# Performance work log

Hardware: AMD Instinct MI355X
Metric: run time of the kernel (lower is better)

The kernel has to match this reference:

```python
import jax, jax.numpy as jnp
import numpy as np

H = 1024  # hidden size
E = 512   # embedding size
L = 2     # lstm layers


def _lstm_cell(x, h, c, W_ih, W_hh, b):
    # x:[B,in], h,c:[B,H]; gates in torch order i,f,g,o
    gates = x @ W_ih.T + h @ W_hh.T + b
    i, f, g, o = jnp.split(gates, 4, axis=-1)
    i, f, o = jax.nn.sigmoid(i), jax.nn.sigmoid(f), jax.nn.sigmoid(o)
    g = jnp.tanh(g)
    c_new = f * c + i * g
    h_new = o * jnp.tanh(c_new)
    return h_new, c_new


def setup_inputs() -> dict:
    key = jax.random.key(0)
    ks = jax.random.split(key, 12)
    B, T, S = 32, 50, 100
    s = 0.02
    return {
        "inputs": jax.random.normal(ks[0], (B, T, E), jnp.float32),
        "memory_bank": jax.random.normal(ks[1], (B, S, H), jnp.float32),
        "mask": jnp.ones((B, S), jnp.bool_),
        "h0": jax.random.normal(ks[2], (L, B, H), jnp.float32),
        "c0": jax.random.normal(ks[3], (L, B, H), jnp.float32),
        "W_ih0": jax.random.normal(ks[4], (4 * H, E + H), jnp.float32) * s,
        "W_hh0": jax.random.normal(ks[5], (4 * H, H), jnp.float32) * s,
        "b0": jnp.zeros((4 * H,), jnp.float32),
        "W_ih1": jax.random.normal(ks[6], (4 * H, H), jnp.float32) * s,
        "W_hh1": jax.random.normal(ks[7], (4 * H, H), jnp.float32) * s,
        "b1": jnp.zeros((4 * H,), jnp.float32),
        "Wa": jax.random.normal(ks[8], (H, H), jnp.float32) * s,
        "Wout": jax.random.normal(ks[9], (H, 2 * H), jnp.float32) * s,
    }


def reference(inputs, memory_bank, mask, h0, c0, W_ih0, W_hh0, b0,
              W_ih1, W_hh1, b1, Wa, Wout):
    B = inputs.shape[0]
    neg = jnp.asarray(-1e9, inputs.dtype)
    # precompute projected memory for general attention: [B,S,H]
    mem_proj = jnp.einsum('bsh,kh->bsk', memory_bank, Wa.T)  # M @ Wa^T later dotted with h

    def step(carry, x_t):
        h, c, feed = carry  # h,c:[L,B,H], feed:[B,H]; x_t:[B,E]
        x = jnp.concatenate([x_t, feed], axis=-1)  # input-feed concat
        h0n, c0n = _lstm_cell(x, h[0], c[0], W_ih0, W_hh0, b0)
        h1n, c1n = _lstm_cell(h0n, h[1], c[1], W_ih1, W_hh1, b1)
        out = h1n  # [B,H]
        # general (Luong) attention
        scores = jnp.einsum('bh,bsh->bs', out @ Wa, memory_bank)  # [B,S]
        scores = jnp.where(mask, scores, neg)
        attn = jax.nn.softmax(scores, axis=-1)
        context = jnp.einsum('bs,bsh->bh', attn, memory_bank)
        o = jnp.tanh(jnp.concatenate([context, out], axis=-1) @ Wout.T)  # [B,H]
        h_new = jnp.stack([h0n, h1n])
        c_new = jnp.stack([c0n, c1n])
        return (h_new, c_new, o), (o, attn)

    feed0 = jnp.zeros((B, H), inputs.dtype)
    (hT, cT, _), (outs, attns) = jax.lax.scan(step, (h0, c0, feed0),
                                              jnp.swapaxes(inputs, 0, 1))
    output_sequences = jnp.swapaxes(outs, 0, 1)   # [B,T,H]
    attentions = jnp.swapaxes(attns, 0, 1)        # [B,T,S]
    return output_sequences, attentions, hT, cT
```

## Files before the change

### kernel.cpp

```cpp
#include <hip/hip_runtime.h>

typedef unsigned short u16;
typedef unsigned int u32;
typedef __attribute__((ext_vector_type(8))) short s8v;
typedef __attribute__((ext_vector_type(4))) float f4v;
typedef __attribute__((ext_vector_type(4))) u16 u16x4;

#define DEVI __device__ __forceinline__

DEVI u16 f2b(float f) {
  u32 u = __float_as_uint(f);
  u32 r = u + 0x7fffu + ((u >> 16) & 1u);
  return (u16)(r >> 16);
}
DEVI float b2f(u16 h) { return __uint_as_float(((u32)h) << 16); }
DEVI f4v mfma16(s8v a, s8v b, f4v c) {
  return __builtin_amdgcn_mfma_f32_16x16x32_bf16(a, b, c, 0, 0, 0);
}
DEVI float sigm(float x) { return 1.0f / (1.0f + __expf(-x)); }

__global__ void k_cvt(const float* __restrict__ src, u16* __restrict__ dst, int n4) {
  int i = blockIdx.x * blockDim.x + threadIdx.x;
  if (i < n4) {
    float4 v = ((const float4*)src)[i];
    u16x4 o = {f2b(v.x), f2b(v.y), f2b(v.z), f2b(v.w)};
    ((u16x4*)dst)[i] = o;
  }
}

__global__ void k_cvt_hl(const float* __restrict__ src, u16* __restrict__ hi,
                         u16* __restrict__ lo, int n4) {
  int i = blockIdx.x * blockDim.x + threadIdx.x;
  if (i < n4) {
    float4 v = ((const float4*)src)[i];
    u16 h0 = f2b(v.x), h1 = f2b(v.y), h2 = f2b(v.z), h3 = f2b(v.w);
    u16x4 oh = {h0, h1, h2, h3};
    u16x4 ol = {f2b(v.x - b2f(h0)), f2b(v.y - b2f(h1)),
                f2b(v.z - b2f(h2)), f2b(v.w - b2f(h3))};
    ((u16x4*)hi)[i] = oh;
    ((u16x4*)lo)[i] = ol;
  }
}

__global__ __launch_bounds__(256) void k_packB(const float* __restrict__ Wa,
                                               const float* __restrict__ Wout,
                                               u16* __restrict__ bh, u16* __restrict__ bl) {
  int r = blockIdx.x;
  const float* src = (r < 1024) ? (Wa + (size_t)r * 1024)
                                : (Wout + (size_t)(r - 1024) * 2048);
  u16* dh = bh + (size_t)r * 1024;
  u16* dl = bl + (size_t)r * 1024;
  for (int c = threadIdx.x * 4; c < 1024; c += 1024) {
    float4 v = *(const float4*)(src + c);
    u16 h0 = f2b(v.x), h1 = f2b(v.y), h2 = f2b(v.z), h3 = f2b(v.w);
    u16x4 oh = {h0, h1, h2, h3};
    u16x4 ol = {f2b(v.x - b2f(h0)), f2b(v.y - b2f(h1)),
                f2b(v.z - b2f(h2)), f2b(v.w - b2f(h3))};
    *(u16x4*)(dh + c) = oh;
    *(u16x4*)(dl + c) = ol;
  }
}

__global__ __launch_bounds__(256) void k_permW(const float* __restrict__ Wih,
                                               const float* __restrict__ Whh,
                                               u16* __restrict__ dst, int Kih, int Khh) {
  int jp = blockIdx.x;
  int u = jp >> 2, g = jp & 3;
  int jsrc = (g << 10) + u;
  int K = Kih + Khh;
  u16* d = dst + (size_t)jp * K;
  const float* s0 = Wih + (size_t)jsrc * Kih;
  const float* s1 = Whh + (size_t)jsrc * Khh;
  for (int k = threadIdx.x * 4; k < Kih; k += 1024) {
    float4 v = *(const float4*)(s0 + k);
    u16x4 o = {f2b(v.x), f2b(v.y), f2b(v.z), f2b(v.w)};
    *(u16x4*)(d + k) = o;
  }
  for (int k = threadIdx.x * 4; k < Khh; k += 1024) {
    float4 v = *(const float4*)(s1 + k);
    u16x4 o = {f2b(v.x), f2b(v.y), f2b(v.z), f2b(v.w)};
    *(u16x4*)(d + Kih + k) = o;
  }
}

#define BKC 128
__global__ __launch_bounds__(256) void k_gemm3c(const float* __restrict__ Af,
                                                const u16* __restrict__ Bh,
                                                const u16* __restrict__ Bl,
                                                float* __restrict__ C,
                                                int M, int N, int K) {
  __shared__ u16 AhL[64 * BKC];
  __shared__ u16 AlL[64 * BKC];
  int nb = N >> 6;
  int rm = blockIdx.x / nb, cn = blockIdx.x - rm * nb;
  int r0 = rm << 6, j0 = cn << 6;
  int tid = threadIdx.x, wave = tid >> 6, lane = tid & 63;
  int rlane = lane & 15, klo = (lane >> 4) << 3;
  f4v acc[4] = {{0, 0, 0, 0}, {0, 0, 0, 0}, {0, 0, 0, 0}, {0, 0, 0, 0}};
  const u16* brh = Bh + (size_t)(j0 + (wave << 4) + rlane) * K + klo;
  const u16* brl = Bl + (size_t)(j0 + (wave << 4) + rlane) * K + klo;

  for (int kc = 0; kc < K; kc += BKC) {
    __syncthreads();
    for (int cidx = tid; cidx < 64 * (BKC / 8); cidx += 256) {
      int row = cidx >> 4;
      int c8 = (cidx & 15) << 3;
      const float* src = Af + (size_t)(r0 + row) * K + kc + c8;
      float4 v0 = *(const float4*)src;
      float4 v1 = *(const float4*)(src + 4);
      float f[8] = {v0.x, v0.y, v0.z, v0.w, v1.x, v1.y, v1.z, v1.w};
      s8v hv, lv;
#pragma unroll
      for (int i = 0; i < 8; ++i) {
        u16 h = f2b(f[i]);
        hv[i] = (short)h;
        lv[i] = (short)f2b(f[i] - b2f(h));
      }
      int boff = ((row * BKC + c8) << 1) ^ ((row & 7) << 4);
      *(s8v*)((char*)AhL + boff) = hv;
      *(s8v*)((char*)AlL + boff) = lv;
    }
    __syncthreads();
#pragma unroll
    for (int ks = 0; ks < BKC; ks += 32) {
      s8v bh = *(const s8v*)(brh + kc + ks);
      s8v bl = *(const s8v*)(brl + kc + ks);
#pragma unroll
      for (int r = 0; r < 4; ++r) {
        int row = (r << 4) + rlane;
        int boff = ((row * BKC + ks + klo) << 1) ^ ((row & 7) << 4);
        s8v ah = *(const s8v*)((char*)AhL + boff);
        s8v al = *(const s8v*)((char*)AlL + boff);
        acc[r] = mfma16(ah, bh, acc[r]);
        acc[r] = mfma16(al, bh, acc[r]);
        acc[r] = mfma16(ah, bl, acc[r]);
      }
    }
  }
  int rr = (lane >> 4) << 2;
  int jc = j0 + (wave << 4) + rlane;
#pragma unroll
  for (int r = 0; r < 4; ++r)
#pragma unroll
    for (int i = 0; i < 4; ++i)
      C[(size_t)(r0 + (r << 4) + rr + i) * N + jc] = acc[r][i];
}

__global__ __launch_bounds__(1024) void k_lstm(
    const u16* __restrict__ a0h, const u16* __restrict__ a0l, int rs0, int kl0,
    const u16* __restrict__ a1h, const u16* __restrict__ a1l, int rs1, int kl1,
    const u16* __restrict__ a2h, const u16* __restrict__ a2l, int rs2, int kl2,
    const u16* __restrict__ W, const float* __restrict__ bias,
    float* __restrict__ c_state, u16* __restrict__ h_hi, u16* __restrict__ h_lo,
    int K) {
  __shared__ float red[8][32][16];
  int wg = blockIdx.x, tid = threadIdx.x;
  int wave = tid >> 6, lane = tid & 63;
  int rlane = lane & 15, klo = (lane >> 4) << 3;
  int kslice = K >> 4;
  int kbeg = wave * kslice, kend = kbeg + kslice;
  f4v acc0 = {0, 0, 0, 0}, acc1 = {0, 0, 0, 0};
  const u16* wrow = W + (size_t)((wg << 4) + rlane) * K;
  const u16* ph[3] = {a0h, a1h, a2h};
  const u16* pl[3] = {a0l, a1l, a2l};
  int rss[3] = {rs0, rs1, rs2};
  int lens[3] = {kl0, kl1, kl2};
  int sstart = 0;
#pragma unroll
  for (int s = 0; s < 3; ++s) {
    int len = lens[s];
    if (len > 0) {
      int lo = kbeg > sstart ? kbeg : sstart;
      int sse = sstart + len;
      int hi = sse < kend ? sse : kend;
      const u16* baseh = ph[s] + klo - sstart;
      const u16* basel = pl[s] + klo - sstart;
      const u16* ah0 = baseh + (size_t)rlane * rss[s];
      const u16* ah1 = baseh + (size_t)(rlane + 16) * rss[s];
      const u16* al0 = basel + (size_t)rlane * rss[s];
      const u16* al1 = basel + (size_t)(rlane + 16) * rss[s];
      for (int k = lo; k < hi; k += 32) {
        s8v b = *(const s8v*)(wrow + k + klo);
        acc0 = mfma16(*(const s8v*)(ah0 + k), b, acc0);
        acc0 = mfma16(*(const s8v*)(al0 + k), b, acc0);
        acc1 = mfma16(*(const s8v*)(ah1 + k), b, acc1);
        acc1 = mfma16(*(const s8v*)(al1 + k), b, acc1);
      }
    }
    sstart += len;
  }
  int rr = (lane >> 4) << 2;
  if (wave < 8) {
#pragma unroll
    for (int i = 0; i < 4; ++i) {
      red[wave][rr + i][rlane] = acc0[i];
      red[wave][16 + rr + i][rlane] = acc1[i];
    }
  }
  __syncthreads();
  if (wave >= 8) {
#pragma unroll
    for (int i = 0; i < 4; ++i) {
      red[wave - 8][rr + i][rlane] += acc0[i];
      red[wave - 8][16 + rr + i][rlane] += acc1[i];
    }
  }
  __syncthreads();
  if (tid < 128) {
    int b = tid & 31, ul = tid >> 5;
    int u = (wg << 2) + ul;
    float g0 = 0, g1 = 0, g2 = 0, g3 = 0;
#pragma unroll
    for (int v = 0; v < 8; ++v) {
      g0 += red[v][b][(ul << 2) + 0];
      g1 += red[v][b][(ul << 2) + 1];
      g2 += red[v][b][(ul << 2) + 2];
      g3 += red[v][b][(ul << 2) + 3];
    }
    float ig = sigm(g0 + bias[u]);
    float fg = sigm(g1 + bias[1024 + u]);
    float gg = tanhf(g2 + bias[2048 + u]);
    float og = sigm(g3 + bias[3072 + u]);
    float c = c_state[(b << 10) + u];
    float cn = fg * c + ig * gg;
    float hn = og * tanhf(cn);
    c_state[(b << 10) + u] = cn;
    u16 hh = f2b(hn);
    h_hi[(b << 10) + u] = hh;
    h_lo[(b << 10) + u] = f2b(hn - b2f(hh));
  }
}

__global__ __launch_bounds__(256) void k_scores(const u16* __restrict__ h1h,
                                                const u16* __restrict__ h1l,
                                                const float* __restrict__ PM,
                                                const u16* __restrict__ WoutB,
                                                float* __restrict__ scores,
                                                float* __restrict__ outpart) {
  __shared__ float red[4][32][16];
  int blk = blockIdx.x, tid = threadIdx.x;
  int wave = tid >> 6, lane = tid & 63;
  if (blk < 128) {
    int b = blk >> 2, sc0 = (blk & 3) * 25;
    const u16* hph = h1h + (b << 10) + (lane << 4);
    const u16* hpl = h1l + (b << 10) + (lane << 4);
    s8v hv0 = *(const s8v*)(hph);
    s8v hv1 = *(const s8v*)(hph + 8);
    s8v lv0 = *(const s8v*)(hpl);
    s8v lv1 = *(const s8v*)(hpl + 8);
    float hv[16];
#pragma unroll
    for (int i = 0; i < 8; ++i) {
      hv[i] = b2f((u16)hv0[i]) + b2f((u16)lv0[i]);
      hv[8 + i] = b2f((u16)hv1[i]) + b2f((u16)lv1[i]);
    }
    for (int si = wave; si < 25; si += 4) {
      int s = sc0 + si;
      const float* mp = PM + ((size_t)(b * 100 + s) << 11) + (lane << 4);
      float acc = 0;
#pragma unroll
      for (int i = 0; i < 16; i += 4) {
        float4 m = *(const float4*)(mp + i);
        acc += hv[i] * m.x + hv[i + 1] * m.y + hv[i + 2] * m.z + hv[i + 3] * m.w;
      }
#pragma unroll
      for (int off = 32; off > 0; off >>= 1) acc += __shfl_xor(acc, off);
      if (lane == 0) scores[b * 100 + s] = acc;
    }
  } else {
    int j0 = (blk - 128) << 4;
    int rlane = lane & 15, klo = (lane >> 4) << 3;
    int kb = wave << 8;
    f4v acc0 = {0, 0, 0, 0}, acc1 = {0, 0, 0, 0};
    const u16* wrow = WoutB + ((size_t)(j0 + rlane) << 11) + 1024 + klo;
    const u16* ah0 = h1h + (rlane << 10) + klo;
    const u16* ah1 = h1h + ((rlane + 16) << 10) + klo;
    const u16* al0 = h1l + (rlane << 10) + klo;
    const u16* al1 = h1l + ((rlane + 16) << 10) + klo;
    for (int k = kb; k < kb + 256; k += 32) {
      s8v b = *(const s8v*)(wrow + k);
      acc0 = mfma16(*(const s8v*)(ah0 + k), b, acc0);
      acc0 = mfma16(*(const s8v*)(al0 + k), b, acc0);
      acc1 = mfma16(*(const s8v*)(ah1 + k), b, acc1);
      acc1 = mfma16(*(const s8v*)(al1 + k), b, acc1);
    }
    int rr = (lane >> 4) << 2;
#pragma unroll
    for (int i = 0; i < 4; ++i) {
      red[wave][rr + i][rlane] = acc0[i];
      red[wave][16 + rr + i][rlane] = acc1[i];
    }
    __syncthreads();
    for (int o = tid; o < 512; o += 256) {
      int bl = o & 31, jl = o >> 5;
      float s = red[0][bl][jl] + red[1][bl][jl] + red[2][bl][jl] + red[3][bl][jl];
      outpart[(bl << 10) + j0 + jl] = s;
    }
  }
}

__global__ __launch_bounds__(256) void k_soft_out(const float* __restrict__ scores,
                                                  const float* __restrict__ PM,
                                                  const float* __restrict__ outpart,
                                                  float* __restrict__ outseq,
                                                  u16* __restrict__ feed_hi,
                                                  u16* __restrict__ feed_lo,
                                                  float* __restrict__ attn_out, int t) {
  __shared__ float sc[100];
  __shared__ float at[104];
  int b = blockIdx.x >> 2, jc = (blockIdx.x & 3) << 8;
  int tid = threadIdx.x;
  if (tid < 100) sc[tid] = scores[b * 100 + tid];
  __syncthreads();
  float m = -1e30f;
  for (int s = 0; s < 100; ++s) m = fmaxf(m, sc[s]);
  float sum = 0;
  for (int s = 0; s < 100; ++s) sum += __expf(sc[s] - m);
  float inv = 1.0f / sum;
  if (tid < 100) {
    float a = __expf(sc[tid] - m) * inv;
    at[tid] = a;
    if ((blockIdx.x & 3) == 0) attn_out[((size_t)b * 50 + t) * 100 + tid] = a;
  }
  __syncthreads();
  int j = jc + tid;
  const float* mo = PM + ((size_t)(b * 100) << 11) + 1024 + j;
  float acc = 0;
  for (int s = 0; s < 100; ++s) acc += at[s] * mo[(size_t)s << 11];
  float val = tanhf(acc + outpart[(b << 10) + j]);
  outseq[((size_t)b * 50 + t) * 1024 + j] = val;
  u16 fh = f2b(val);
  feed_hi[(b << 10) + j] = fh;
  feed_lo[(b << 10) + j] = f2b(val - b2f(fh));
}

__global__ void k_init(const float* __restrict__ h0, const float* __restrict__ c0,
                       u16* __restrict__ h0h, u16* __restrict__ h0l,
                       u16* __restrict__ h1h, u16* __restrict__ h1l,
                       float* __restrict__ cs0, float* __restrict__ cs1,
                       u16* __restrict__ feed_hi, u16* __restrict__ feed_lo) {
  int i = blockIdx.x * blockDim.x + threadIdx.x;
  if (i < 32768) {
    float v0 = h0[i], v1 = h0[32768 + i];
    u16 a = f2b(v0), b = f2b(v1);
    h0h[i] = a;
    h0l[i] = f2b(v0 - b2f(a));
    h1h[i] = b;
    h1l[i] = f2b(v1 - b2f(b));
    cs0[i] = c0[i];
    cs1[i] = c0[32768 + i];
    feed_hi[i] = 0;
    feed_lo[i] = 0;
  }
}

__global__ void k_final(const u16* __restrict__ h0h, const u16* __restrict__ h0l,
                        const u16* __restrict__ h1h, const u16* __restrict__ h1l,
                        const float* __restrict__ cs0, const float* __restrict__ cs1,
                        float* __restrict__ out_hT, float* __restrict__ out_cT) {
  int i = blockIdx.x * blockDim.x + threadIdx.x;
  if (i < 32768) {
    out_hT[i] = b2f(h0h[i]) + b2f(h0l[i]);
    out_hT[32768 + i] = b2f(h1h[i]) + b2f(h1l[i]);
    out_cT[i] = cs0[i];
    out_cT[32768 + i] = cs1[i];
  }
}

extern "C" void kernel_launch(void* const* d_in, const int* in_sizes, int n_in,
                              void* d_out, int out_size, void* d_ws, size_t ws_size,
                              hipStream_t stream) {
  const float* inputs = (const float*)d_in[0];
  const float* membank = (const float*)d_in[1];
  const float* h0 = (const float*)d_in[3];
  const float* c0 = (const float*)d_in[4];
  const float* W_ih0 = (const float*)d_in[5];
  const float* W_hh0 = (const float*)d_in[6];
  const float* b0 = (const float*)d_in[7];
  const float* W_ih1 = (const float*)d_in[8];
  const float* W_hh1 = (const float*)d_in[9];
  const float* b1 = (const float*)d_in[10];
  const float* Wa = (const float*)d_in[11];
  const float* Wout = (const float*)d_in[12];

  char* p = (char*)d_ws;
  auto take = [&](size_t bytes) {
    char* r = p;
    p += (bytes + 255) & ~(size_t)255;
    return r;
  };
  u16* in_hi = (u16*)take((size_t)819200 * 2);
  u16* in_lo = (u16*)take((size_t)819200 * 2);
  u16* Bc_hi = (u16*)take((size_t)2048 * 1024 * 2);
  u16* Bc_lo = (u16*)take((size_t)2048 * 1024 * 2);
  u16* Wout_bf = (u16*)take((size_t)2097152 * 2);
  u16* Wb0p = (u16*)take((size_t)4096 * 2560 * 2);
  u16* Wb1p = (u16*)take((size_t)4096 * 2048 * 2);
  float* PM = (float*)take((size_t)3200 * 2048 * 4);
  u16* h0hA = (u16*)take(32768 * 2);
  u16* h0lA = (u16*)take(32768 * 2);
  u16* h0hB = (u16*)take(32768 * 2);
  u16* h0lB = (u16*)take(32768 * 2);
  u16* h1hA = (u16*)take(32768 * 2);
  u16* h1lA = (u16*)take(32768 * 2);
  u16* h1hB = (u16*)take(32768 * 2);
  u16* h1lB = (u16*)take(32768 * 2);
  float* cs0 = (float*)take(32768 * 4);
  float* cs1 = (float*)take(32768 * 4);
  u16* feed_hi = (u16*)take(32768 * 2);
  u16* feed_lo = (u16*)take(32768 * 2);
  float* scoresb = (float*)take(3200 * 4);
  float* outpart = (float*)take(32768 * 4);

  k_cvt_hl<<<800, 256, 0, stream>>>(inputs, in_hi, in_lo, 204800);
  k_cvt<<<2048, 256, 0, stream>>>(Wout, Wout_bf, 524288);
  k_packB<<<2048, 256, 0, stream>>>(Wa, Wout, Bc_hi, Bc_lo);
  k_permW<<<4096, 256, 0, stream>>>(W_ih0, W_hh0, Wb0p, 1536, 1024);
  k_permW<<<4096, 256, 0, stream>>>(W_ih1, W_hh1, Wb1p, 1024, 1024);
  k_gemm3c<<<50 * 32, 256, 0, stream>>>(membank, Bc_hi, Bc_lo, PM,
                                        3200, 2048, 1024);
  k_init<<<128, 256, 0, stream>>>(h0, c0, h0hA, h0lA, h1hA, h1lA, cs0, cs1,
                                  feed_hi, feed_lo);

  float* outseq = (float*)d_out;
  float* attn_out = outseq + 1638400;
  float* out_hT = attn_out + 160000;
  float* out_cT = out_hT + 65536;

  u16* h0h[2] = {h0hA, h0hB};
  u16* h0l[2] = {h0lA, h0lB};
  u16* h1h[2] = {h1hA, h1hB};
  u16* h1l[2] = {h1lA, h1lB};
  for (int t = 0; t < 50; ++t) {
    int pi = t & 1, po = pi ^ 1;
    k_lstm<<<256, 1024, 0, stream>>>(in_hi + t * 512, in_lo + t * 512, 25600, 512,
                                     feed_hi, feed_lo, 1024, 1024,
                                     h0h[pi], h0l[pi], 1024, 1024,
                                     Wb0p, b0, cs0, h0h[po], h0l[po], 2560);
    k_lstm<<<256, 1024, 0, stream>>>(h0h[po], h0l[po], 1024, 1024,
                                     h1h[pi], h1l[pi], 1024, 1024,
                                     (const u16*)nullptr, (const u16*)nullptr, 0, 0,
                                     Wb1p, b1, cs1, h1h[po], h1l[po], 2048);
    k_scores<<<192, 256, 0, stream>>>(h1h[po], h1l[po], PM, Wout_bf,
                                      scoresb, outpart);
    k_soft_out<<<128, 256, 0, stream>>>(scoresb, PM, outpart, outseq,
                                        feed_hi, feed_lo, attn_out, t);
  }
  k_final<<<128, 256, 0, stream>>>(h0h[0], h0l[0], h1h[0], h1l[0], cs0, cs1,
                                   out_hT, out_cT);
}
```

Baseline: 2.065 ms.

## Hoist input-to-gate projection out of recurrence into one batched GEMM

The x_t part of the layer-0 gate matmul is now computed for all timesteps up front by a single batched split-bf16 GEMM into a gates_x buffer. Each per-step LSTM kernel adds that precomputed slice instead of running MFMAs over the 512 input columns, so the K of the recurrent matmul drops from 2560 to 2048. The memory-bank projection used for the output is now stored as bf16 in a narrower array, and the GEMM block order is remapped per XCD for locality. The gates_x buffer adds a large fp32 read per step, and bf16 storage of the output projection lowers precision.

```diff
diff --git a/kernel.cpp b/kernel.cpp
--- a/kernel.cpp
+++ b/kernel.cpp
@@ -18,29 +18,6 @@
   return __builtin_amdgcn_mfma_f32_16x16x32_bf16(a, b, c, 0, 0, 0);
 }
 DEVI float sigm(float x) { return 1.0f / (1.0f + __expf(-x)); }
-
-__global__ void k_cvt(const float* __restrict__ src, u16* __restrict__ dst, int n4) {
-  int i = blockIdx.x * blockDim.x + threadIdx.x;
-  if (i < n4) {
-    float4 v = ((const float4*)src)[i];
-    u16x4 o = {f2b(v.x), f2b(v.y), f2b(v.z), f2b(v.w)};
-    ((u16x4*)dst)[i] = o;
-  }
-}
-
-__global__ void k_cvt_hl(const float* __restrict__ src, u16* __restrict__ hi,
-                         u16* __restrict__ lo, int n4) {
-  int i = blockIdx.x * blockDim.x + threadIdx.x;
-  if (i < n4) {
-    float4 v = ((const float4*)src)[i];
-    u16 h0 = f2b(v.x), h1 = f2b(v.y), h2 = f2b(v.z), h3 = f2b(v.w);
-    u16x4 oh = {h0, h1, h2, h3};
-    u16x4 ol = {f2b(v.x - b2f(h0)), f2b(v.y - b2f(h1)),
-                f2b(v.z - b2f(h2)), f2b(v.w - b2f(h3))};
-    ((u16x4*)hi)[i] = oh;
-    ((u16x4*)lo)[i] = ol;
-  }
-}
 
 __global__ __launch_bounds__(256) void k_packB(const float* __restrict__ Wa,
                                                const float* __restrict__ Wout,
@@ -61,38 +38,62 @@
   }
 }
 
-__global__ __launch_bounds__(256) void k_permW(const float* __restrict__ Wih,
-                                               const float* __restrict__ Whh,
-                                               u16* __restrict__ dst, int Kih, int Khh) {
+__global__ __launch_bounds__(256) void k_packR(const float* __restrict__ Wout,
+                                               u16* __restrict__ dst) {
+  int r = blockIdx.x;
+  for (int c = threadIdx.x * 4; c < 1024; c += 1024) {
+    float4 v = *(const float4*)(Wout + (size_t)r * 2048 + 1024 + c);
+    u16x4 o = {f2b(v.x), f2b(v.y), f2b(v.z), f2b(v.w)};
+    *(u16x4*)(dst + (size_t)r * 1024 + c) = o;
+  }
+}
+
+__global__ __launch_bounds__(256) void k_permW2(const float* __restrict__ S0, int stride0, int len0,
+                                                const float* __restrict__ S1, int stride1, int len1,
+                                                u16* __restrict__ dh, u16* __restrict__ dl) {
   int jp = blockIdx.x;
   int u = jp >> 2, g = jp & 3;
   int jsrc = (g << 10) + u;
-  int K = Kih + Khh;
-  u16* d = dst + (size_t)jp * K;
-  const float* s0 = Wih + (size_t)jsrc * Kih;
-  const float* s1 = Whh + (size_t)jsrc * Khh;
-  for (int k = threadIdx.x * 4; k < Kih; k += 1024) {
-    float4 v = *(const float4*)(s0 + k);
-    u16x4 o = {f2b(v.x), f2b(v.y), f2b(v.z), f2b(v.w)};
-    *(u16x4*)(d + k) = o;
-  }
-  for (int k = threadIdx.x * 4; k < Khh; k += 1024) {
-    float4 v = *(const float4*)(s1 + k);
-    u16x4 o = {f2b(v.x), f2b(v.y), f2b(v.z), f2b(v.w)};
-    *(u16x4*)(d + Kih + k) = o;
+  int K = len0 + len1;
+  u16* outh = dh + (size_t)jp * K;
+  u16* outl = dl ? dl + (size_t)jp * K : nullptr;
+  const float* srcs[2] = {S0 ? S0 + (size_t)jsrc * stride0 : nullptr,
+                          S1 ? S1 + (size_t)jsrc * stride1 : nullptr};
+  int lens[2] = {len0, len1};
+  int off = 0;
+#pragma unroll
+  for (int s = 0; s < 2; ++s) {
+    if (lens[s] > 0) {
+      for (int k = threadIdx.x * 4; k < lens[s]; k += 1024) {
+        float4 v = *(const float4*)(srcs[s] + k);
+        u16 h0 = f2b(v.x), h1 = f2b(v.y), h2 = f2b(v.z), h3 = f2b(v.w);
+        u16x4 oh = {h0, h1, h2, h3};
+        *(u16x4*)(outh + off + k) = oh;
+        if (outl) {
+          u16x4 ol = {f2b(v.x - b2f(h0)), f2b(v.y - b2f(h1)),
+                      f2b(v.z - b2f(h2)), f2b(v.w - b2f(h3))};
+          *(u16x4*)(outl + off + k) = ol;
+        }
+      }
+    }
+    off += lens[s];
   }
 }
 
 #define BKC 128
+template <int MODE>
 __global__ __launch_bounds__(256) void k_gemm3c(const float* __restrict__ Af,
                                                 const u16* __restrict__ Bh,
                                                 const u16* __restrict__ Bl,
-                                                float* __restrict__ C,
-                                                int M, int N, int K) {
+                                                float* __restrict__ Cf,
+                                                u16* __restrict__ Cb,
+                                                int N, int K, int cnPerXcd) {
   __shared__ u16 AhL[64 * BKC];
   __shared__ u16 AlL[64 * BKC];
-  int nb = N >> 6;
-  int rm = blockIdx.x / nb, cn = blockIdx.x - rm * nb;
+  int bid = blockIdx.x;
+  int xcd = bid & 7, jj = bid >> 3;
+  int cn = xcd * cnPerXcd + (jj % cnPerXcd);
+  int rm = jj / cnPerXcd;
   int r0 = rm << 6, j0 = cn << 6;
   int tid = threadIdx.x, wave = tid >> 6, lane = tid & 63;
   int rlane = lane & 15, klo = (lane >> 4) << 3;
@@ -139,18 +140,34 @@
   }
   int rr = (lane >> 4) << 2;
   int jc = j0 + (wave << 4) + rlane;
-#pragma unroll
-  for (int r = 0; r < 4; ++r)
-#pragma unroll
-    for (int i = 0; i < 4; ++i)
-      C[(size_t)(r0 + (r << 4) + rr + i) * N + jc] = acc[r][i];
+  if (MODE == 0) {
+#pragma unroll
+    for (int r = 0; r < 4; ++r)
+#pragma unroll
+      for (int i = 0; i < 4; ++i)
+        Cf[(size_t)(r0 + (r << 4) + rr + i) * N + jc] = acc[r][i];
+  } else {
+    if (j0 < 1024) {
+#pragma unroll
+      for (int r = 0; r < 4; ++r)
+#pragma unroll
+        for (int i = 0; i < 4; ++i)
+          Cf[((size_t)(r0 + (r << 4) + rr + i) << 10) + jc] = acc[r][i];
+    } else {
+#pragma unroll
+      for (int r = 0; r < 4; ++r)
+#pragma unroll
+        for (int i = 0; i < 4; ++i)
+          Cb[((size_t)(r0 + (r << 4) + rr + i) << 10) + jc - 1024] = f2b(acc[r][i]);
+    }
+  }
 }
 
 __global__ __launch_bounds__(1024) void k_lstm(
     const u16* __restrict__ a0h, const u16* __restrict__ a0l, int rs0, int kl0,
     const u16* __restrict__ a1h, const u16* __restrict__ a1l, int rs1, int kl1,
-    const u16* __restrict__ a2h, const u16* __restrict__ a2l, int rs2, int kl2,
     const u16* __restrict__ W, const float* __restrict__ bias,
+    const float* __restrict__ gx,
     float* __restrict__ c_state, u16* __restrict__ h_hi, u16* __restrict__ h_lo,
     int K) {
   __shared__ float red[8][32][16];
@@ -161,13 +178,13 @@
   int kbeg = wave * kslice, kend = kbeg + kslice;
   f4v acc0 = {0, 0, 0, 0}, acc1 = {0, 0, 0, 0};
   const u16* wrow = W + (size_t)((wg << 4) + rlane) * K;
-  const u16* ph[3] = {a0h, a1h, a2h};
-  const u16* pl[3] = {a0l, a1l, a2l};
-  int rss[3] = {rs0, rs1, rs2};
-  int lens[3] = {kl0, kl1, kl2};
+  const u16* ph[2] = {a0h, a1h};
+  const u16* pl[2] = {a0l, a1l};
+  int rss[2] = {rs0, rs1};
+  int lens[2] = {kl0, kl1};
   int sstart = 0;
 #pragma unroll
-  for (int s = 0; s < 3; ++s) {
+  for (int s = 0; s < 2; ++s) {
     int len = lens[s];
     if (len > 0) {
       int lo = kbeg > sstart ? kbeg : sstart;
@@ -217,6 +234,13 @@
       g2 += red[v][b][(ul << 2) + 2];
       g3 += red[v][b][(ul << 2) + 3];
     }
+    if (gx) {
+      float4 gv = *(const float4*)(gx + (size_t)b * 204800 + ((size_t)u << 2));
+      g0 += gv.x;
+      g1 += gv.y;
+      g2 += gv.z;
+      g3 += gv.w;
+    }
     float ig = sigm(g0 + bias[u]);
     float fg = sigm(g1 + bias[1024 + u]);
     float gg = tanhf(g2 + bias[2048 + u]);
@@ -233,8 +257,8 @@
 
 __global__ __launch_bounds__(256) void k_scores(const u16* __restrict__ h1h,
                                                 const u16* __restrict__ h1l,
-                                                const float* __restrict__ PM,
-                                                const u16* __restrict__ WoutB,
+                                                const float* __restrict__ MP,
+                                                const u16* __restrict__ WoutR,
                                                 float* __restrict__ scores,
                                                 float* __restrict__ outpart) {
   __shared__ float red[4][32][16];
@@ -256,7 +280,7 @@
     }
     for (int si = wave; si < 25; si += 4) {
       int s = sc0 + si;
-      const float* mp = PM + ((size_t)(b * 100 + s) << 11) + (lane << 4);
+      const float* mp = MP + ((size_t)(b * 100 + s) << 10) + (lane << 4);
       float acc = 0;
 #pragma unroll
       for (int i = 0; i < 16; i += 4) {
@@ -272,7 +296,7 @@
     int rlane = lane & 15, klo = (lane >> 4) << 3;
     int kb = wave << 8;
     f4v acc0 = {0, 0, 0, 0}, acc1 = {0, 0, 0, 0};
-    const u16* wrow = WoutB + ((size_t)(j0 + rlane) << 11) + 1024 + klo;
+    const u16* wrow = WoutR + ((size_t)(j0 + rlane) << 10) + klo;
     const u16* ah0 = h1h + (rlane << 10) + klo;
     const u16* ah1 = h1h + ((rlane + 16) << 10) + klo;
     const u16* al0 = h1l + (rlane << 10) + klo;
@@ -300,7 +324,7 @@
 }
 
 __global__ __launch_bounds__(256) void k_soft_out(const float* __restrict__ scores,
-                                                  const float* __restrict__ PM,
+                                                  const u16* __restrict__ MO,
                                                   const float* __restrict__ outpart,
                                                   float* __restrict__ outseq,
                                                   u16* __restrict__ feed_hi,
@@ -324,9 +348,9 @@
   }
   __syncthreads();
   int j = jc + tid;
-  const float* mo = PM + ((size_t)(b * 100) << 11) + 1024 + j;
+  const u16* mo = MO + ((size_t)(b * 100) << 10) + j;
   float acc = 0;
-  for (int s = 0; s < 100; ++s) acc += at[s] * mo[(size_t)s << 11];
+  for (int s = 0; s < 100; ++s) acc += at[s] * b2f(mo[(size_t)s << 10]);
   float val = tanhf(acc + outpart[(b << 10) + j]);
   outseq[((size_t)b * 50 + t) * 1024 + j] = val;
   u16 fh = f2b(val);
@@ -389,14 +413,16 @@
     p += (bytes + 255) & ~(size_t)255;
     return r;
   };
-  u16* in_hi = (u16*)take((size_t)819200 * 2);
-  u16* in_lo = (u16*)take((size_t)819200 * 2);
   u16* Bc_hi = (u16*)take((size_t)2048 * 1024 * 2);
   u16* Bc_lo = (u16*)take((size_t)2048 * 1024 * 2);
-  u16* Wout_bf = (u16*)take((size_t)2097152 * 2);
-  u16* Wb0p = (u16*)take((size_t)4096 * 2560 * 2);
+  u16* WoutR = (u16*)take((size_t)1024 * 1024 * 2);
+  u16* Wx_hi = (u16*)take((size_t)4096 * 512 * 2);
+  u16* Wx_lo = (u16*)take((size_t)4096 * 512 * 2);
+  u16* Wb0rec = (u16*)take((size_t)4096 * 2048 * 2);
   u16* Wb1p = (u16*)take((size_t)4096 * 2048 * 2);
-  float* PM = (float*)take((size_t)3200 * 2048 * 4);
+  float* MP = (float*)take((size_t)3200 * 1024 * 4);
+  u16* MO = (u16*)take((size_t)3200 * 1024 * 2);
+  float* gates_x = (float*)take((size_t)1600 * 4096 * 4);
   u16* h0hA = (u16*)take(32768 * 2);
   u16* h0lA = (u16*)take(32768 * 2);
   u16* h0hB = (u16*)take(32768 * 2);
@@ -412,13 +438,17 @@
   float* scoresb = (float*)take(3200 * 4);
   float* outpart = (float*)take(32768 * 4);
 
-  k_cvt_hl<<<800, 256, 0, stream>>>(inputs, in_hi, in_lo, 204800);
-  k_cvt<<<2048, 256, 0, stream>>>(Wout, Wout_bf, 524288);
   k_packB<<<2048, 256, 0, stream>>>(Wa, Wout, Bc_hi, Bc_lo);
-  k_permW<<<4096, 256, 0, stream>>>(W_ih0, W_hh0, Wb0p, 1536, 1024);
-  k_permW<<<4096, 256, 0, stream>>>(W_ih1, W_hh1, Wb1p, 1024, 1024);
-  k_gemm3c<<<50 * 32, 256, 0, stream>>>(membank, Bc_hi, Bc_lo, PM,
-                                        3200, 2048, 1024);
+  k_packR<<<1024, 256, 0, stream>>>(Wout, WoutR);
+  k_permW2<<<4096, 256, 0, stream>>>(W_ih0, 1536, 512, (const float*)nullptr, 0, 0,
+                                     Wx_hi, Wx_lo);
+  k_permW2<<<4096, 256, 0, stream>>>(W_ih0 + 512, 1536, 1024, W_hh0, 1024, 1024,
+                                     Wb0rec, (u16*)nullptr);
+  k_permW2<<<4096, 256, 0, stream>>>(W_ih1, 1024, 1024, W_hh1, 1024, 1024,
+                                     Wb1p, (u16*)nullptr);
+  k_gemm3c<1><<<1600, 256, 0, stream>>>(membank, Bc_hi, Bc_lo, MP, MO, 2048, 1024, 4);
+  k_gemm3c<0><<<1600, 256, 0, stream>>>(inputs, Wx_hi, Wx_lo, gates_x, (u16*)nullptr,
+                                        4096, 512, 8);
   k_init<<<128, 256, 0, stream>>>(h0, c0, h0hA, h0lA, h1hA, h1lA, cs0, cs1,
                                   feed_hi, feed_lo);
 
@@ -433,17 +463,17 @@
   u16* h1l[2] = {h1lA, h1lB};
   for (int t = 0; t < 50; ++t) {
     int pi = t & 1, po = pi ^ 1;
-    k_lstm<<<256, 1024, 0, stream>>>(in_hi + t * 512, in_lo + t * 512, 25600, 512,
-                                     feed_hi, feed_lo, 1024, 1024,
+    k_lstm<<<256, 1024, 0, stream>>>(feed_hi, feed_lo, 1024, 1024,
                                      h0h[pi], h0l[pi], 1024, 1024,
-                                     Wb0p, b0, cs0, h0h[po], h0l[po], 2560);
+                                     Wb0rec, b0, gates_x + (size_t)t * 4096,
+                                     cs0, h0h[po], h0l[po], 2048);
     k_lstm<<<256, 1024, 0, stream>>>(h0h[po], h0l[po], 1024, 1024,
                                      h1h[pi], h1l[pi], 1024, 1024,
-                                     (const u16*)nullptr, (const u16*)nullptr, 0, 0,
-                                     Wb1p, b1, cs1, h1h[po], h1l[po], 2048);
-    k_scores<<<192, 256, 0, stream>>>(h1h[po], h1l[po], PM, Wout_bf,
+                                     Wb1p, b1, (const float*)nullptr,
+                                     cs1, h1h[po], h1l[po], 2048);
+    k_scores<<<192, 256, 0, stream>>>(h1h[po], h1l[po], MP, WoutR,
                                       scoresb, outpart);
-    k_soft_out<<<128, 256, 0, stream>>>(scoresb, PM, outpart, outseq,
+    k_soft_out<<<128, 256, 0, stream>>>(scoresb, MO, outpart, outseq,
                                         feed_hi, feed_lo, attn_out, t);
   }
   k_final<<<128, 256, 0, stream>>>(h0h[0], h0l[0], h1h[0], h1l[0], cs0, cs1,
```

Result: slower. 2.146 ms (+3.9%).

## Split projected memory into fp32 scores and bf16 output planes; XCD-aware GEMM tiling

Applied to the files above, without the earlier changes.

The precomputed memory projection is split into two contiguous buffers: an fp32 [3200x1024] plane for attention scores and a bf16 [3200x1024] plane for the context-times-Wout product. This halves the stride and bytes read by the per-step soft_out kernel, which now also uses two accumulators. The unused half of Wout is packed into a dense 1024x1024 array, which drops the full Wout conversion. The setup GEMM remaps block IDs so that column tiles are grouped per XCD for L2 reuse. Storing the output plane in bf16 reduces precision in the context projection.

```diff
diff --git a/kernel.cpp b/kernel.cpp
--- a/kernel.cpp
+++ b/kernel.cpp
@@ -18,15 +18,6 @@
   return __builtin_amdgcn_mfma_f32_16x16x32_bf16(a, b, c, 0, 0, 0);
 }
 DEVI float sigm(float x) { return 1.0f / (1.0f + __expf(-x)); }
-
-__global__ void k_cvt(const float* __restrict__ src, u16* __restrict__ dst, int n4) {
-  int i = blockIdx.x * blockDim.x + threadIdx.x;
-  if (i < n4) {
-    float4 v = ((const float4*)src)[i];
-    u16x4 o = {f2b(v.x), f2b(v.y), f2b(v.z), f2b(v.w)};
-    ((u16x4*)dst)[i] = o;
-  }
-}
 
 __global__ void k_cvt_hl(const float* __restrict__ src, u16* __restrict__ hi,
                          u16* __restrict__ lo, int n4) {
@@ -61,6 +52,16 @@
   }
 }
 
+__global__ __launch_bounds__(256) void k_packR(const float* __restrict__ Wout,
+                                               u16* __restrict__ dst) {
+  int r = blockIdx.x;
+  for (int c = threadIdx.x * 4; c < 1024; c += 1024) {
+    float4 v = *(const float4*)(Wout + (size_t)r * 2048 + 1024 + c);
+    u16x4 o = {f2b(v.x), f2b(v.y), f2b(v.z), f2b(v.w)};
+    *(u16x4*)(dst + (size_t)r * 1024 + c) = o;
+  }
+}
+
 __global__ __launch_bounds__(256) void k_permW(const float* __restrict__ Wih,
                                                const float* __restrict__ Whh,
                                                u16* __restrict__ dst, int Kih, int Khh) {
@@ -87,12 +88,15 @@
 __global__ __launch_bounds__(256) void k_gemm3c(const float* __restrict__ Af,
                                                 const u16* __restrict__ Bh,
                                                 const u16* __restrict__ Bl,
-                                                float* __restrict__ C,
-                                                int M, int N, int K) {
+                                                float* __restrict__ Cf,
+                                                u16* __restrict__ Cb,
+                                                int N, int K, int cnPerXcd) {
   __shared__ u16 AhL[64 * BKC];
   __shared__ u16 AlL[64 * BKC];
-  int nb = N >> 6;
-  int rm = blockIdx.x / nb, cn = blockIdx.x - rm * nb;
+  int bid = blockIdx.x;
+  int xcd = bid & 7, jj = bid >> 3;
+  int cn = xcd * cnPerXcd + (jj % cnPerXcd);
+  int rm = jj / cnPerXcd;
   int r0 = rm << 6, j0 = cn << 6;
   int tid = threadIdx.x, wave = tid >> 6, lane = tid & 63;
   int rlane = lane & 15, klo = (lane >> 4) << 3;
@@ -126,24 +130,32 @@
       s8v bh = *(const s8v*)(brh + kc + ks);
       s8v bl = *(const s8v*)(brl + kc + ks);
 #pragma unroll
-      for (int r = 0; r < 4; ++r) {
-        int row = (r << 4) + rlane;
+      for (int rr2 = 0; rr2 < 4; ++rr2) {
+        int row = (rr2 << 4) + rlane;
         int boff = ((row * BKC + ks + klo) << 1) ^ ((row & 7) << 4);
         s8v ah = *(const s8v*)((char*)AhL + boff);
         s8v al = *(const s8v*)((char*)AlL + boff);
-        acc[r] = mfma16(ah, bh, acc[r]);
-        acc[r] = mfma16(al, bh, acc[r]);
-        acc[r] = mfma16(ah, bl, acc[r]);
+        acc[rr2] = mfma16(ah, bh, acc[rr2]);
+        acc[rr2] = mfma16(al, bh, acc[rr2]);
+        acc[rr2] = mfma16(ah, bl, acc[rr2]);
       }
     }
   }
   int rr = (lane >> 4) << 2;
   int jc = j0 + (wave << 4) + rlane;
-#pragma unroll
-  for (int r = 0; r < 4; ++r)
-#pragma unroll
-    for (int i = 0; i < 4; ++i)
-      C[(size_t)(r0 + (r << 4) + rr + i) * N + jc] = acc[r][i];
+  if (j0 < 1024) {
+#pragma unroll
+    for (int q = 0; q < 4; ++q)
+#pragma unroll
+      for (int i = 0; i < 4; ++i)
+        Cf[((size_t)(r0 + (q << 4) + rr + i) << 10) + jc] = acc[q][i];
+  } else {
+#pragma unroll
+    for (int q = 0; q < 4; ++q)
+#pragma unroll
+      for (int i = 0; i < 4; ++i)
+        Cb[((size_t)(r0 + (q << 4) + rr + i) << 10) + jc - 1024] = f2b(acc[q][i]);
+  }
 }
 
 __global__ __launch_bounds__(1024) void k_lstm(
@@ -233,8 +245,8 @@
 
 __global__ __launch_bounds__(256) void k_scores(const u16* __restrict__ h1h,
                                                 const u16* __restrict__ h1l,
-                                                const float* __restrict__ PM,
-                                                const u16* __restrict__ WoutB,
+                                                const float* __restrict__ MP,
+                                                const u16* __restrict__ WoutR,
                                                 float* __restrict__ scores,
                                                 float* __restrict__ outpart) {
   __shared__ float red[4][32][16];
@@ -256,7 +268,7 @@
     }
     for (int si = wave; si < 25; si += 4) {
       int s = sc0 + si;
-      const float* mp = PM + ((size_t)(b * 100 + s) << 11) + (lane << 4);
+      const float* mp = MP + ((size_t)(b * 100 + s) << 10) + (lane << 4);
       float acc = 0;
 #pragma unroll
       for (int i = 0; i < 16; i += 4) {
@@ -272,7 +284,7 @@
     int rlane = lane & 15, klo = (lane >> 4) << 3;
     int kb = wave << 8;
     f4v acc0 = {0, 0, 0, 0}, acc1 = {0, 0, 0, 0};
-    const u16* wrow = WoutB + ((size_t)(j0 + rlane) << 11) + 1024 + klo;
+    const u16* wrow = WoutR + ((size_t)(j0 + rlane) << 10) + klo;
     const u16* ah0 = h1h + (rlane << 10) + klo;
     const u16* ah1 = h1h + ((rlane + 16) << 10) + klo;
     const u16* al0 = h1l + (rlane << 10) + klo;
@@ -300,7 +312,7 @@
 }
 
 __global__ __launch_bounds__(256) void k_soft_out(const float* __restrict__ scores,
-                                                  const float* __restrict__ PM,
+                                                  const u16* __restrict__ MO,
                                                   const float* __restrict__ outpart,
                                                   float* __restrict__ outseq,
                                                   u16* __restrict__ feed_hi,
@@ -324,10 +336,14 @@
   }
   __syncthreads();
   int j = jc + tid;
-  const float* mo = PM + ((size_t)(b * 100) << 11) + 1024 + j;
-  float acc = 0;
-  for (int s = 0; s < 100; ++s) acc += at[s] * mo[(size_t)s << 11];
-  float val = tanhf(acc + outpart[(b << 10) + j]);
+  const u16* mo = MO + ((size_t)(b * 100) << 10) + j;
+  float accA = 0, accB = 0;
+#pragma unroll 4
+  for (int s = 0; s < 100; s += 2) {
+    accA += at[s] * b2f(mo[(size_t)s << 10]);
+    accB += at[s + 1] * b2f(mo[(size_t)(s + 1) << 10]);
+  }
+  float val = tanhf(accA + accB + outpart[(b << 10) + j]);
   outseq[((size_t)b * 50 + t) * 1024 + j] = val;
   u16 fh = f2b(val);
   feed_hi[(b << 10) + j] = fh;
@@ -393,10 +409,11 @@
   u16* in_lo = (u16*)take((size_t)819200 * 2);
   u16* Bc_hi = (u16*)take((size_t)2048 * 1024 * 2);
   u16* Bc_lo = (u16*)take((size_t)2048 * 1024 * 2);
-  u16* Wout_bf = (u16*)take((size_t)2097152 * 2);
+  u16* WoutR = (u16*)take((size_t)1024 * 1024 * 2);
   u16* Wb0p = (u16*)take((size_t)4096 * 2560 * 2);
   u16* Wb1p = (u16*)take((size_t)4096 * 2048 * 2);
-  float* PM = (float*)take((size_t)3200 * 2048 * 4);
+  float* MP = (float*)take((size_t)3200 * 1024 * 4);
+  u16* MO = (u16*)take((size_t)3200 * 1024 * 2);
   u16* h0hA = (u16*)take(32768 * 2);
   u16* h0lA = (u16*)take(32768 * 2);
   u16* h0hB = (u16*)take(32768 * 2);
@@ -413,12 +430,11 @@
   float* outpart = (float*)take(32768 * 4);
 
   k_cvt_hl<<<800, 256, 0, stream>>>(inputs, in_hi, in_lo, 204800);
-  k_cvt<<<2048, 256, 0, stream>>>(Wout, Wout_bf, 524288);
   k_packB<<<2048, 256, 0, stream>>>(Wa, Wout, Bc_hi, Bc_lo);
+  k_packR<<<1024, 256, 0, stream>>>(Wout, WoutR);
   k_permW<<<4096, 256, 0, stream>>>(W_ih0, W_hh0, Wb0p, 1536, 1024);
   k_permW<<<4096, 256, 0, stream>>>(W_ih1, W_hh1, Wb1p, 1024, 1024);
-  k_gemm3c<<<50 * 32, 256, 0, stream>>>(membank, Bc_hi, Bc_lo, PM,
-                                        3200, 2048, 1024);
+  k_gemm3c<<<1600, 256, 0, stream>>>(membank, Bc_hi, Bc_lo, MP, MO, 2048, 1024, 4);
   k_init<<<128, 256, 0, stream>>>(h0, c0, h0hA, h0lA, h1hA, h1lA, cs0, cs1,
                                   feed_hi, feed_lo);
 
@@ -441,9 +457,9 @@
                                      h1h[pi], h1l[pi], 1024, 1024,
                                      (const u16*)nullptr, (const u16*)nullptr, 0, 0,
                                      Wb1p, b1, cs1, h1h[po], h1l[po], 2048);
-    k_scores<<<192, 256, 0, stream>>>(h1h[po], h1l[po], PM, Wout_bf,
+    k_scores<<<192, 256, 0, stream>>>(h1h[po], h1l[po], MP, WoutR,
                                       scoresb, outpart);
-    k_soft_out<<<128, 256, 0, stream>>>(scoresb, PM, outpart, outseq,
+    k_soft_out<<<128, 256, 0, stream>>>(scoresb, MO, outpart, outseq,
                                         feed_hi, feed_lo, attn_out, t);
   }
   k_final<<<128, 256, 0, stream>>>(h0h[0], h0l[0], h1h[0], h1l[0], cs0, cs1,
```

Result: slower. 2.316 ms (+12.1%).
